# Kernel tuning notes

Measured on AMD Instinct MI355X. Metric: run time of the kernel, lower is better.

## Reference

```python
import jax, jax.numpy as jnp
import numpy as np

B, N, NODE_DIM, HID_DIM = 64, 4096, 128, 128
D = NODE_DIM + HID_DIM  # concat of ndata['h'] and ndata['x']


def setup_inputs() -> dict:
    key = jax.random.key(0)
    k1, k2, k3, k4 = jax.random.split(key, 4)
    feats = jax.random.normal(k1, (B, N, D), dtype=jnp.float32)
    # per-graph node counts in [1, N] (split_batch asserts size != 0)
    node_counts = jax.random.randint(k2, (B,), 1, N + 1, dtype=jnp.int32)
    Wi = jax.random.normal(k3, (D, 1), dtype=jnp.float32) * 0.05   # project_i weight
    bi = jnp.zeros((1,), dtype=jnp.float32)
    Wj = jax.random.normal(k4, (D, HID_DIM), dtype=jnp.float32) * 0.05  # project_j weight
    bj = jnp.zeros((HID_DIM,), dtype=jnp.float32)
    return {"feats": feats, "node_counts": node_counts,
            "Wi": Wi, "bi": bi, "Wj": Wj, "bj": bj}


def reference(feats, node_counts, Wi, bi, Wj, bj):
    # mask: True at padded node slots (equivalent to zero-pad + sum==0 in split_batch)
    n = feats.shape[1]
    mask = jnp.arange(n)[None, :] >= node_counts[:, None]          # [B, N]
    feats = jnp.where(mask[..., None], 0.0, feats)                  # zero padding rows
    scores = feats @ Wi + bi                                        # [B, N, 1]
    scores = jnp.where(mask[..., None], -100000.0, scores)          # masked_fill
    h1 = jax.nn.softmax(scores, axis=1)                             # softmax over nodes
    h2 = feats @ Wj + bj                                            # [B, N, HID_DIM]
    return jnp.einsum('bni,bnj->bj', h1, h2)                        # [B, HID_DIM]
```

## Files before the change

### kernel.cpp

```cpp
#include <hip/hip_runtime.h>


#define NDIM 256
#define HID 128
#define NMAX 4096
#define ROWS_PER_BLK 160
#define NCHUNK 26
#define PSTRIDE 260
#define FLAG_MAGIC 0x5EED5EEDu

__global__ __launch_bounds__(512) void pool_fused(
    const float* __restrict__ feats, const int* __restrict__ counts,
    const float* __restrict__ Wi, const float* __restrict__ bi,
    const float* __restrict__ Wj, const float* __restrict__ bj,
    unsigned int* __restrict__ flags, float* __restrict__ part_g,
    float* __restrict__ out)
{
    const int b     = blockIdx.y;
    const int count = counts[b];
    const int tid   = threadIdx.x;
    const int nch   = (count + ROWS_PER_BLK - 1) / ROWS_PER_BLK;

    __shared__ float lds_acc[8][NDIM];
    __shared__ float lds_l[8];
    __shared__ float red[2][NDIM];
    __shared__ float redl[2];
    __shared__ float pooled[NDIM];
    __shared__ float tmp[4][HID];

    if (blockIdx.x < NCHUNK) {
        const int row0 = blockIdx.x * ROWS_PER_BLK;
        if (row0 >= count) return;
        const int row_end = min(row0 + ROWS_PER_BLK, count);

        const int lane = tid & 63;
        const int wv   = tid >> 6;
        const int g    = lane >> 4;
        const int q    = lane & 15;

        const float4* Wi4 = reinterpret_cast<const float4*>(Wi);
        const float4 wi0 = Wi4[q], wi1 = Wi4[16 + q], wi2 = Wi4[32 + q], wi3 = Wi4[48 + q];
        const float  fbi = bi[0];

        const float* fb = feats + (size_t)b * NMAX * NDIM;

        float4 a0 = {0,0,0,0}, a1 = {0,0,0,0}, a2 = {0,0,0,0}, a3 = {0,0,0,0};
        float lsum = 0.f;

        const int wbase = row0 + wv * 20;
        #pragma unroll
        for (int it = 0; it < 5; ++it) {
            const int r = wbase + it * 4 + g;
            const bool valid = (r < row_end);
            float4 f0 = {0,0,0,0}, f1 = {0,0,0,0}, f2 = {0,0,0,0}, f3 = {0,0,0,0};
            if (valid) {
                const float4* rp = reinterpret_cast<const float4*>(fb + (size_t)r * NDIM);
                f0 = rp[q]; f1 = rp[16 + q]; f2 = rp[32 + q]; f3 = rp[48 + q];
            }
            float sp = f0.x*wi0.x + f0.y*wi0.y + f0.z*wi0.z + f0.w*wi0.w
                     + f1.x*wi1.x + f1.y*wi1.y + f1.z*wi1.z + f1.w*wi1.w
                     + f2.x*wi2.x + f2.y*wi2.y + f2.z*wi2.z + f2.w*wi2.w
                     + f3.x*wi3.x + f3.y*wi3.y + f3.z*wi3.z + f3.w*wi3.w;
            sp += __shfl_xor(sp, 1, 64);
            sp += __shfl_xor(sp, 2, 64);
            sp += __shfl_xor(sp, 4, 64);
            sp += __shfl_xor(sp, 8, 64);
            const float w = valid ? __expf(sp + fbi) : 0.f;
            lsum += w;
            a0.x += w*f0.x; a0.y += w*f0.y; a0.z += w*f0.z; a0.w += w*f0.w;
            a1.x += w*f1.x; a1.y += w*f1.y; a1.z += w*f1.z; a1.w += w*f1.w;
            a2.x += w*f2.x; a2.y += w*f2.y; a2.z += w*f2.z; a2.w += w*f2.w;
            a3.x += w*f3.x; a3.y += w*f3.y; a3.z += w*f3.z; a3.w += w*f3.w;
        }

        #define COMB(x) x += __shfl_xor(x, 16, 64); x += __shfl_xor(x, 32, 64)
        COMB(a0.x); COMB(a0.y); COMB(a0.z); COMB(a0.w);
        COMB(a1.x); COMB(a1.y); COMB(a1.z); COMB(a1.w);
        COMB(a2.x); COMB(a2.y); COMB(a2.z); COMB(a2.w);
        COMB(a3.x); COMB(a3.y); COMB(a3.z); COMB(a3.w);
        COMB(lsum);
        #undef COMB

        if (g == 0) {
            float* dst = &lds_acc[wv][0];
            *reinterpret_cast<float4*>(&dst[q*4      ]) = a0;
            *reinterpret_cast<float4*>(&dst[q*4 +  64]) = a1;
            *reinterpret_cast<float4*>(&dst[q*4 + 128]) = a2;
            *reinterpret_cast<float4*>(&dst[q*4 + 192]) = a3;
            if (q == 0) lds_l[wv] = lsum;
        }
        __syncthreads();

        float* part = part_g + (size_t)(b * NCHUNK + blockIdx.x) * PSTRIDE;
        if (tid < NDIM) {
            float v = 0.f;
            #pragma unroll
            for (int k = 0; k < 8; ++k) v += lds_acc[k][tid];
            __hip_atomic_store(&part[tid], v, __ATOMIC_RELAXED,
                               __HIP_MEMORY_SCOPE_AGENT);
        } else if (tid == NDIM) {
            float v = 0.f;
            #pragma unroll
            for (int k = 0; k < 8; ++k) v += lds_l[k];
            __hip_atomic_store(&part[NDIM], v, __ATOMIC_RELAXED,
                               __HIP_MEMORY_SCOPE_AGENT);
        }
        __syncthreads();
        if (tid == 0)
            __hip_atomic_store(&flags[b * NCHUNK + blockIdx.x], FLAG_MAGIC,
                               __ATOMIC_RELAXED, __HIP_MEMORY_SCOPE_AGENT);
        return;
    }

    if (tid < 64) {
        for (int c = 0; c < nch; ++c) {
            while (__hip_atomic_load(&flags[b * NCHUNK + c], __ATOMIC_RELAXED,
                                     __HIP_MEMORY_SCOPE_AGENT) != FLAG_MAGIC)
                __builtin_amdgcn_s_sleep(2);
        }
    }
    asm volatile("" ::: "memory");
    __syncthreads();

    const int t    = tid & (NDIM - 1);
    const int half = tid >> 8;
    float acc = 0.f, l = 0.f;
    for (int c = half; c < nch; c += 2) {
        float* p = part_g + (size_t)(b * NCHUNK + c) * PSTRIDE;
        acc += __hip_atomic_load(&p[t],    __ATOMIC_RELAXED, __HIP_MEMORY_SCOPE_AGENT);
        l   += __hip_atomic_load(&p[NDIM], __ATOMIC_RELAXED, __HIP_MEMORY_SCOPE_AGENT);
    }
    red[half][t] = acc;
    if (t == 0) redl[half] = l;
    __syncthreads();
    if (tid < NDIM)
        pooled[tid] = (red[0][tid] + red[1][tid]) / (redl[0] + redl[1]);
    __syncthreads();

    const int j  = tid & (HID - 1);
    const int ks = (tid >> 7) * 64;
    float s = 0.f;
    #pragma unroll 16
    for (int k = 0; k < 64; ++k)
        s += pooled[ks + k] * Wj[(ks + k) * HID + j];
    tmp[tid >> 7][j] = s;
    __syncthreads();
    if (tid < HID)
        out[b * HID + tid] = tmp[0][tid] + tmp[1][tid] + tmp[2][tid]
                           + tmp[3][tid] + bj[tid];
}

extern "C" void kernel_launch(void* const* d_in, const int* in_sizes, int n_in,
                              void* d_out, int out_size, void* d_ws, size_t ws_size,
                              hipStream_t stream) {
    const float* feats  = (const float*)d_in[0];
    const int*   counts = (const int*)  d_in[1];
    const float* Wi     = (const float*)d_in[2];
    const float* bi     = (const float*)d_in[3];
    const float* Wj     = (const float*)d_in[4];
    const float* bj     = (const float*)d_in[5];
    float* out = (float*)d_out;

    const int B = in_sizes[1];

    unsigned int* flags  = (unsigned int*)d_ws;
    float*        part_g = (float*)d_ws + B * NCHUNK;

    dim3 g1(NCHUNK + 1, B);
    pool_fused<<<g1, 512, 0, stream>>>(feats, counts, Wi, bi, Wj, bj,
                                       flags, part_g, out);
}
```

Baseline: 29.15 us.

## Replace spin-wait consumer blocks with persistent work-stealing and last-block finalize

Switches from a 2D grid that has a dedicated spinning consumer block per graph to a persistent grid of 1024 blocks. These blocks pull (graph, chunk) tiles from a global atomic cursor, interleaved across graphs. A per-graph atomic done-counter lets the last finishing chunk block do the reduction and the Wj projection, so no block spins waiting for flags. This removes the idle spinning consumers and empty early-exit blocks, but adds a hipMemsetAsync per call and an atomic per tile. The new ordering also relies on relaxed atomics with no explicit release/acquire fence.

```diff
diff --git a/kernel.cpp b/kernel.cpp
--- a/kernel.cpp
+++ b/kernel.cpp
@@ -7,19 +7,22 @@
 #define ROWS_PER_BLK 160
 #define NCHUNK 26
 #define PSTRIDE 260
-#define FLAG_MAGIC 0x5EED5EEDu
+#define NGRAPH 64
+#define NTICK (NGRAPH * NCHUNK)
+#define NPROD 1024
 
-__global__ __launch_bounds__(512) void pool_fused(
+__global__ __launch_bounds__(512) void pool_ws(
     const float* __restrict__ feats, const int* __restrict__ counts,
     const float* __restrict__ Wi, const float* __restrict__ bi,
     const float* __restrict__ Wj, const float* __restrict__ bj,
-    unsigned int* __restrict__ flags, float* __restrict__ part_g,
-    float* __restrict__ out)
+    unsigned int* __restrict__ cursor, unsigned int* __restrict__ done,
+    float* __restrict__ part_g, float* __restrict__ out)
 {
-    const int b     = blockIdx.y;
-    const int count = counts[b];
-    const int tid   = threadIdx.x;
-    const int nch   = (count + ROWS_PER_BLK - 1) / ROWS_PER_BLK;
+    const int tid  = threadIdx.x;
+    const int lane = tid & 63;
+    const int wv   = tid >> 6;
+    const int g    = lane >> 4;
+    const int q    = lane & 15;
 
     __shared__ float lds_acc[8][NDIM];
     __shared__ float lds_l[8];
@@ -27,127 +30,127 @@
     __shared__ float redl[2];
     __shared__ float pooled[NDIM];
     __shared__ float tmp[4][HID];
+    __shared__ unsigned int s_tick;
+    __shared__ unsigned int s_old;
 
-    if (blockIdx.x < NCHUNK) {
-        const int row0 = blockIdx.x * ROWS_PER_BLK;
-        if (row0 >= count) return;
-        const int row_end = min(row0 + ROWS_PER_BLK, count);
+    const float4* Wi4 = reinterpret_cast<const float4*>(Wi);
+    const float4 wi0 = Wi4[q], wi1 = Wi4[16 + q], wi2 = Wi4[32 + q], wi3 = Wi4[48 + q];
+    const float  fbi = bi[0];
 
-        const int lane = tid & 63;
-        const int wv   = tid >> 6;
-        const int g    = lane >> 4;
-        const int q    = lane & 15;
+    unsigned int t = blockIdx.x;
 
-        const float4* Wi4 = reinterpret_cast<const float4*>(Wi);
-        const float4 wi0 = Wi4[q], wi1 = Wi4[16 + q], wi2 = Wi4[32 + q], wi3 = Wi4[48 + q];
-        const float  fbi = bi[0];
+    while (t < NTICK) {
+        const int b     = (int)(t & (NGRAPH - 1));
+        const int c     = (int)(t >> 6);
+        const int count = counts[b];
+        const int row0  = c * ROWS_PER_BLK;
 
-        const float* fb = feats + (size_t)b * NMAX * NDIM;
+        if (row0 < count) {
+            const int row_end = min(row0 + ROWS_PER_BLK, count);
+            const float* fb = feats + (size_t)b * NMAX * NDIM;
 
-        float4 a0 = {0,0,0,0}, a1 = {0,0,0,0}, a2 = {0,0,0,0}, a3 = {0,0,0,0};
-        float lsum = 0.f;
+            float4 a0 = {0,0,0,0}, a1 = {0,0,0,0}, a2 = {0,0,0,0}, a3 = {0,0,0,0};
+            float lsum = 0.f;
 
-        const int wbase = row0 + wv * 20;
-        #pragma unroll
-        for (int it = 0; it < 5; ++it) {
-            const int r = wbase + it * 4 + g;
-            const bool valid = (r < row_end);
-            float4 f0 = {0,0,0,0}, f1 = {0,0,0,0}, f2 = {0,0,0,0}, f3 = {0,0,0,0};
-            if (valid) {
-                const float4* rp = reinterpret_cast<const float4*>(fb + (size_t)r * NDIM);
-                f0 = rp[q]; f1 = rp[16 + q]; f2 = rp[32 + q]; f3 = rp[48 + q];
+            const int wbase = row0 + wv * 20;
+            #pragma unroll
+            for (int it = 0; it < 5; ++it) {
+                const int r = wbase + it * 4 + g;
+                const bool valid = (r < row_end);
+                float4 f0 = {0,0,0,0}, f1 = {0,0,0,0}, f2 = {0,0,0,0}, f3 = {0,0,0,0};
+                if (valid) {
+                    const float4* rp = reinterpret_cast<const float4*>(fb + (size_t)r * NDIM);
+                    f0 = rp[q]; f1 = rp[16 + q]; f2 = rp[32 + q]; f3 = rp[48 + q];
+                }
+                float sp = f0.x*wi0.x + f0.y*wi0.y + f0.z*wi0.z + f0.w*wi0.w
+                         + f1.x*wi1.x + f1.y*wi1.y + f1.z*wi1.z + f1.w*wi1.w
+                         + f2.x*wi2.x + f2.y*wi2.y + f2.z*wi2.z + f2.w*wi2.w
+                         + f3.x*wi3.x + f3.y*wi3.y + f3.z*wi3.z + f3.w*wi3.w;
+                sp += __shfl_xor(sp, 1, 64);
+                sp += __shfl_xor(sp, 2, 64);
+                sp += __shfl_xor(sp, 4, 64);
+                sp += __shfl_xor(sp, 8, 64);
+                const float w = valid ? __expf(sp + fbi) : 0.f;
+                lsum += w;
+                a0.x += w*f0.x; a0.y += w*f0.y; a0.z += w*f0.z; a0.w += w*f0.w;
+                a1.x += w*f1.x; a1.y += w*f1.y; a1.z += w*f1.z; a1.w += w*f1.w;
+                a2.x += w*f2.x; a2.y += w*f2.y; a2.z += w*f2.z; a2.w += w*f2.w;
+                a3.x += w*f3.x; a3.y += w*f3.y; a3.z += w*f3.z; a3.w += w*f3.w;
             }
-            float sp = f0.x*wi0.x + f0.y*wi0.y + f0.z*wi0.z + f0.w*wi0.w
-                     + f1.x*wi1.x + f1.y*wi1.y + f1.z*wi1.z + f1.w*wi1.w
-                     + f2.x*wi2.x + f2.y*wi2.y + f2.z*wi2.z + f2.w*wi2.w
-                     + f3.x*wi3.x + f3.y*wi3.y + f3.z*wi3.z + f3.w*wi3.w;
-            sp += __shfl_xor(sp, 1, 64);
-            sp += __shfl_xor(sp, 2, 64);
-            sp += __shfl_xor(sp, 4, 64);
-            sp += __shfl_xor(sp, 8, 64);
-            const float w = valid ? __expf(sp + fbi) : 0.f;
-            lsum += w;
-            a0.x += w*f0.x; a0.y += w*f0.y; a0.z += w*f0.z; a0.w += w*f0.w;
-            a1.x += w*f1.x; a1.y += w*f1.y; a1.z += w*f1.z; a1.w += w*f1.w;
-            a2.x += w*f2.x; a2.y += w*f2.y; a2.z += w*f2.z; a2.w += w*f2.w;
-            a3.x += w*f3.x; a3.y += w*f3.y; a3.z += w*f3.z; a3.w += w*f3.w;
+
+            #define COMB(x) x += __shfl_xor(x, 16, 64); x += __shfl_xor(x, 32, 64)
+            COMB(a0.x); COMB(a0.y); COMB(a0.z); COMB(a0.w);
+            COMB(a1.x); COMB(a1.y); COMB(a1.z); COMB(a1.w);
+            COMB(a2.x); COMB(a2.y); COMB(a2.z); COMB(a2.w);
+            COMB(a3.x); COMB(a3.y); COMB(a3.z); COMB(a3.w);
+            COMB(lsum);
+            #undef COMB
+
+            if (g == 0) {
+                float* dst = &lds_acc[wv][0];
+                *reinterpret_cast<float4*>(&dst[q*4      ]) = a0;
+                *reinterpret_cast<float4*>(&dst[q*4 +  64]) = a1;
+                *reinterpret_cast<float4*>(&dst[q*4 + 128]) = a2;
+                *reinterpret_cast<float4*>(&dst[q*4 + 192]) = a3;
+                if (q == 0) lds_l[wv] = lsum;
+            }
+            __syncthreads();
+
+            float* part = part_g + (size_t)(b * NCHUNK + c) * PSTRIDE;
+            if (tid < NDIM) {
+                float v = 0.f;
+                #pragma unroll
+                for (int k = 0; k < 8; ++k) v += lds_acc[k][tid];
+                __hip_atomic_store(&part[tid], v, __ATOMIC_RELAXED,
+                                   __HIP_MEMORY_SCOPE_AGENT);
+            } else if (tid == NDIM) {
+                float v = 0.f;
+                #pragma unroll
+                for (int k = 0; k < 8; ++k) v += lds_l[k];
+                __hip_atomic_store(&part[NDIM], v, __ATOMIC_RELAXED,
+                                   __HIP_MEMORY_SCOPE_AGENT);
+            }
+            __syncthreads();
+            if (tid == 0) s_old = atomicAdd(&done[b], 1u);
+            __syncthreads();
+
+            const int nch = (count + ROWS_PER_BLK - 1) / ROWS_PER_BLK;
+            if ((int)s_old == nch - 1) {
+                asm volatile("" ::: "memory");
+                const int tt   = tid & (NDIM - 1);
+                const int half = tid >> 8;
+                float acc = 0.f, l = 0.f;
+                for (int cc = half; cc < nch; cc += 2) {
+                    float* p = part_g + (size_t)(b * NCHUNK + cc) * PSTRIDE;
+                    acc += __hip_atomic_load(&p[tt],   __ATOMIC_RELAXED, __HIP_MEMORY_SCOPE_AGENT);
+                    l   += __hip_atomic_load(&p[NDIM], __ATOMIC_RELAXED, __HIP_MEMORY_SCOPE_AGENT);
+                }
+                red[half][tt] = acc;
+                if (tt == 0) redl[half] = l;
+                __syncthreads();
+                if (tid < NDIM)
+                    pooled[tid] = (red[0][tid] + red[1][tid]) / (redl[0] + redl[1]);
+                __syncthreads();
+
+                const int j  = tid & (HID - 1);
+                const int ks = (tid >> 7) * 64;
+                float s = 0.f;
+                #pragma unroll 16
+                for (int k = 0; k < 64; ++k)
+                    s += pooled[ks + k] * Wj[(ks + k) * HID + j];
+                tmp[tid >> 7][j] = s;
+                __syncthreads();
+                if (tid < HID)
+                    out[b * HID + tid] = tmp[0][tid] + tmp[1][tid] + tmp[2][tid]
+                                       + tmp[3][tid] + bj[tid];
+            }
         }
 
-        #define COMB(x) x += __shfl_xor(x, 16, 64); x += __shfl_xor(x, 32, 64)
-        COMB(a0.x); COMB(a0.y); COMB(a0.z); COMB(a0.w);
-        COMB(a1.x); COMB(a1.y); COMB(a1.z); COMB(a1.w);
-        COMB(a2.x); COMB(a2.y); COMB(a2.z); COMB(a2.w);
-        COMB(a3.x); COMB(a3.y); COMB(a3.z); COMB(a3.w);
-        COMB(lsum);
-        #undef COMB
-
-        if (g == 0) {
-            float* dst = &lds_acc[wv][0];
-            *reinterpret_cast<float4*>(&dst[q*4      ]) = a0;
-            *reinterpret_cast<float4*>(&dst[q*4 +  64]) = a1;
-            *reinterpret_cast<float4*>(&dst[q*4 + 128]) = a2;
-            *reinterpret_cast<float4*>(&dst[q*4 + 192]) = a3;
-            if (q == 0) lds_l[wv] = lsum;
-        }
         __syncthreads();
-
-        float* part = part_g + (size_t)(b * NCHUNK + blockIdx.x) * PSTRIDE;
-        if (tid < NDIM) {
-            float v = 0.f;
-            #pragma unroll
-            for (int k = 0; k < 8; ++k) v += lds_acc[k][tid];
-            __hip_atomic_store(&part[tid], v, __ATOMIC_RELAXED,
-                               __HIP_MEMORY_SCOPE_AGENT);
-        } else if (tid == NDIM) {
-            float v = 0.f;
-            #pragma unroll
-            for (int k = 0; k < 8; ++k) v += lds_l[k];
-            __hip_atomic_store(&part[NDIM], v, __ATOMIC_RELAXED,
-                               __HIP_MEMORY_SCOPE_AGENT);
-        }
+        if (tid == 0) s_tick = atomicAdd(cursor, 1u) + NPROD;
         __syncthreads();
-        if (tid == 0)
-            __hip_atomic_store(&flags[b * NCHUNK + blockIdx.x], FLAG_MAGIC,
-                               __ATOMIC_RELAXED, __HIP_MEMORY_SCOPE_AGENT);
-        return;
+        t = s_tick;
     }
-
-    if (tid < 64) {
-        for (int c = 0; c < nch; ++c) {
-            while (__hip_atomic_load(&flags[b * NCHUNK + c], __ATOMIC_RELAXED,
-                                     __HIP_MEMORY_SCOPE_AGENT) != FLAG_MAGIC)
-                __builtin_amdgcn_s_sleep(2);
-        }
-    }
-    asm volatile("" ::: "memory");
-    __syncthreads();
-
-    const int t    = tid & (NDIM - 1);
-    const int half = tid >> 8;
-    float acc = 0.f, l = 0.f;
-    for (int c = half; c < nch; c += 2) {
-        float* p = part_g + (size_t)(b * NCHUNK + c) * PSTRIDE;
-        acc += __hip_atomic_load(&p[t],    __ATOMIC_RELAXED, __HIP_MEMORY_SCOPE_AGENT);
-        l   += __hip_atomic_load(&p[NDIM], __ATOMIC_RELAXED, __HIP_MEMORY_SCOPE_AGENT);
-    }
-    red[half][t] = acc;
-    if (t == 0) redl[half] = l;
-    __syncthreads();
-    if (tid < NDIM)
-        pooled[tid] = (red[0][tid] + red[1][tid]) / (redl[0] + redl[1]);
-    __syncthreads();
-
-    const int j  = tid & (HID - 1);
-    const int ks = (tid >> 7) * 64;
-    float s = 0.f;
-    #pragma unroll 16
-    for (int k = 0; k < 64; ++k)
-        s += pooled[ks + k] * Wj[(ks + k) * HID + j];
-    tmp[tid >> 7][j] = s;
-    __syncthreads();
-    if (tid < HID)
-        out[b * HID + tid] = tmp[0][tid] + tmp[1][tid] + tmp[2][tid]
-                           + tmp[3][tid] + bj[tid];
 }
 
 extern "C" void kernel_launch(void* const* d_in, const int* in_sizes, int n_in,
@@ -161,12 +164,12 @@
     const float* bj     = (const float*)d_in[5];
     float* out = (float*)d_out;
 
-    const int B = in_sizes[1];
+    unsigned int* cursor = (unsigned int*)d_ws;
+    unsigned int* done   = (unsigned int*)((char*)d_ws + 256);
+    float*        part_g = (float*)((char*)d_ws + 512);
 
-    unsigned int* flags  = (unsigned int*)d_ws;
-    float*        part_g = (float*)d_ws + B * NCHUNK;
+    hipMemsetAsync(d_ws, 0, 512, stream);
 
-    dim3 g1(NCHUNK + 1, B);
-    pool_fused<<<g1, 512, 0, stream>>>(feats, counts, Wi, bi, Wj, bj,
-                                       flags, part_g, out);
+    pool_ws<<<NPROD, 512, 0, stream>>>(feats, counts, Wi, bi, Wj, bj,
+                                       cursor, done, part_g, out);
 }
```

Measured after the change: 47.42 us. 1.63x slower.
